# Kernel tuning notes

Hardware: AMD Instinct MI355X
Metric: run time of the kernel (lower is better)

Reference implementation:

```python
import jax, jax.numpy as jnp
from jax import lax
import numpy as np

TOP_PERCENT = 1.3
KSIZE = 3
SIGMA = 0.3 * ((KSIZE - 1) * 0.5 - 1) + 0.8  # torchvision default sigma for ksize=3 -> 0.8


def _gaussian_kernel1d():
    x = jnp.arange(KSIZE, dtype=jnp.float32) - (KSIZE - 1) / 2.0
    k = jnp.exp(-0.5 * (x / SIGMA) ** 2)
    return k / k.sum()


def setup_inputs() -> dict:
    key = jax.random.key(0)
    img = jax.random.uniform(key, (3, 4096, 4096), dtype=jnp.float32)
    return {"img": img}


def reference(img):
    # --- rgb_to_grayscale (ITU-R 601 coefficients, as torchvision) ---
    gray = 0.2989 * img[0] + 0.587 * img[1] + 0.114 * img[2]  # [H, W]

    # --- separable 3x3 gaussian blur, reflect padding (torchvision) ---
    k = _gaussian_kernel1d()
    p = jnp.pad(gray, 1, mode="reflect")  # [H+2, W+2]
    # horizontal pass
    h = k[0] * p[:, :-2] + k[1] * p[:, 1:-1] + k[2] * p[:, 2:]  # [H+2, W]
    # vertical pass
    blur = k[0] * h[:-2, :] + k[1] * h[1:-1, :] + k[2] * h[2:, :]  # [H, W]

    # --- quantile threshold (linear interpolation, matches torch.quantile) ---
    q = (100.0 - TOP_PERCENT) / 100.0
    threshold = jnp.quantile(blur, q)
    mask = (blur >= threshold).astype(jnp.int32)  # [H, W]

    # --- binary opening with 5x5 ones footprint ---
    # erosion = min filter; outside-image treated as 0 (scipy border_value=0),
    # so pad explicitly with zeros and reduce with VALID windows.
    INT_MAX = np.iinfo(np.int32).max
    INT_MIN = np.iinfo(np.int32).min
    padded = jnp.pad(mask, 2)  # zero pad -> borders erode
    eroded = lax.reduce_window(padded, INT_MAX, lax.min, (5, 5), (1, 1), "VALID")
    # dilation = max filter; identity padding (-inf equiv) matches border_value=0
    opened = lax.reduce_window(eroded, INT_MIN, lax.max, (5, 5), (1, 1), "SAME")

    return opened[None, :, :].astype(jnp.int32)  # [1, H, W]
```

## Files before the change

### kernel.cpp

```cpp
#include <hip/hip_runtime.h>
#include <stdint.h>
#include <cmath>


#define HH 4096
#define WW 4096
#define NPIX 16777216u
#define KRANK 16559111u
#define TW 128
#define TH 32

__device__ __forceinline__ unsigned ukey(float v) {
  return (unsigned)(v * 268435456.0f);
}

__global__ __launch_bounds__(256) void k_blur_hist(const float* __restrict__ img,
    float* __restrict__ blur, unsigned* __restrict__ hist1,
    float kn0, float kn1) {
  __shared__ float g[TH + 2][TW + 2];
  __shared__ float hb[TH + 2][TW];
  __shared__ unsigned hist[4096];
  const int tid = threadIdx.x;
  for (int i = tid; i < 4096; i += 256) hist[i] = 0u;

  const int bx = blockIdx.x & 31;
  const int by = blockIdx.x >> 5;
  const int c0 = bx * TW, r0 = by * TH;
  const float* __restrict__ Rp = img;
  const float* __restrict__ Gp = img + (size_t)NPIX;
  const float* __restrict__ Bp = img + 2 * (size_t)NPIX;

  for (int idx = tid; idx < (TH + 2) * (TW + 2); idx += 256) {
    int row = idx / (TW + 2), col = idx - row * (TW + 2);
    int gr = r0 - 1 + row, gc = c0 - 1 + col;
    gr = (gr < 0) ? -gr : ((gr > HH - 1) ? (2 * (HH - 1) - gr) : gr);
    gc = (gc < 0) ? -gc : ((gc > WW - 1) ? (2 * (WW - 1) - gc) : gc);
    size_t o = (size_t)gr * WW + gc;
    float gray = __fadd_rn(__fadd_rn(__fmul_rn(0.2989f, Rp[o]),
                                     __fmul_rn(0.587f, Gp[o])),
                           __fmul_rn(0.114f, Bp[o]));
    g[row][col] = gray;
  }
  __syncthreads();

  for (int idx = tid; idx < (TH + 2) * TW; idx += 256) {
    int row = idx / TW, col = idx - row * TW;
    hb[row][col] = __fadd_rn(__fadd_rn(__fmul_rn(kn0, g[row][col]),
                                       __fmul_rn(kn1, g[row][col + 1])),
                             __fmul_rn(kn0, g[row][col + 2]));
  }
  __syncthreads();

  for (int idx = tid; idx < TH * TW; idx += 256) {
    int row = idx / TW, col = idx - row * TW;
    float v = __fadd_rn(__fadd_rn(__fmul_rn(kn0, hb[row][col]),
                                  __fmul_rn(kn1, hb[row + 1][col])),
                        __fmul_rn(kn0, hb[row + 2][col]));
    blur[(size_t)(r0 + row) * WW + (c0 + col)] = v;
    atomicAdd(&hist[ukey(v) >> 16], 1u);
  }
  __syncthreads();
  for (int i = tid; i < 4096; i += 256) {
    unsigned c = hist[i];
    if (c) atomicAdd(&hist1[i], c);
  }
}

__global__ __launch_bounds__(256) void k_sel1(const unsigned* __restrict__ hist1,
                                              unsigned* __restrict__ sel) {
  __shared__ unsigned part[256];
  const int t = threadIdx.x;
  unsigned loc[16];
  unsigned s = 0;
  for (int i = 0; i < 16; ++i) { loc[i] = hist1[t * 16 + i]; s += loc[i]; }
  part[t] = s;
  __syncthreads();
  for (int off = 1; off < 256; off <<= 1) {
    unsigned v = (t >= off) ? part[t - off] : 0u;
    __syncthreads();
    part[t] += v;
    __syncthreads();
  }
  unsigned incl = part[t], excl = incl - s;
  if (excl <= KRANK && KRANK < incl) {
    unsigned p = excl;
    for (int i = 0; i < 16; ++i) {
      if (KRANK < p + loc[i]) { sel[0] = (unsigned)(t * 16 + i); sel[1] = KRANK - p; break; }
      p += loc[i];
    }
  }
}

__global__ __launch_bounds__(256) void k_hist2(const float4* __restrict__ blur4,
    const unsigned* __restrict__ sel, unsigned* __restrict__ hist2) {
  const unsigned b1 = sel[0];
  size_t i = (size_t)blockIdx.x * 256 + threadIdx.x;
  float4 v = blur4[i];
  unsigned u;
  u = ukey(v.x); if ((u >> 16) == b1) atomicAdd(&hist2[u & 0xFFFFu], 1u);
  u = ukey(v.y); if ((u >> 16) == b1) atomicAdd(&hist2[u & 0xFFFFu], 1u);
  u = ukey(v.z); if ((u >> 16) == b1) atomicAdd(&hist2[u & 0xFFFFu], 1u);
  u = ukey(v.w); if ((u >> 16) == b1) atomicAdd(&hist2[u & 0xFFFFu], 1u);
}

__global__ __launch_bounds__(1024) void k_sel2(const unsigned* __restrict__ hist2,
    const unsigned* __restrict__ sel, float* __restrict__ tptr) {
  __shared__ unsigned part[1024];
  const int t = threadIdx.x;
  const unsigned base = (unsigned)t * 64u;
  unsigned s = 0;
  for (int i = 0; i < 64; ++i) s += hist2[base + i];
  part[t] = s;
  __syncthreads();
  for (int off = 1; off < 1024; off <<= 1) {
    unsigned v = (t >= off) ? part[t - off] : 0u;
    __syncthreads();
    part[t] += v;
    __syncthreads();
  }
  unsigned incl = part[t], excl = incl - s;
  unsigned b1 = sel[0], r1 = sel[1];
  if (excl <= r1 && r1 < incl) {
    unsigned p = excl;
    for (int i = 0; i < 64; ++i) {
      unsigned c = hist2[base + i];
      if (r1 < p + c) {
        unsigned long long ustar = ((unsigned long long)b1 << 16) | (base + i);
        double vv = (double)ustar * (1.0 / 268435456.0);
        *tptr = (float)vv;
        break;
      }
      p += c;
    }
  }
}

__global__ __launch_bounds__(256) void k_mask(const float* __restrict__ blur,
    const float* __restrict__ tptr, unsigned long long* __restrict__ mbits) {
  size_t i = (size_t)blockIdx.x * 256 + threadIdx.x;
  float T = *tptr;
  unsigned long long w = __ballot(blur[i] >= T);
  if ((threadIdx.x & 63) == 0) mbits[i >> 6] = w;
}

__global__ __launch_bounds__(256) void k_erode(
    const unsigned long long* __restrict__ mbits,
    unsigned long long* __restrict__ ebits) {
  int w = blockIdx.x * 256 + threadIdx.x;
  int r = w >> 6, wc = w & 63;
  unsigned long long acc = ~0ull;
  for (int dr = -2; dr <= 2; ++dr) {
    int rr = r + dr;
    unsigned long long h = 0ull;
    if (rr >= 0 && rr <= HH - 1) {
      int rb = (rr << 6) + wc;
      unsigned long long C = mbits[rb];
      unsigned long long L = (wc > 0) ? mbits[rb - 1] : 0ull;
      unsigned long long R = (wc < 63) ? mbits[rb + 1] : 0ull;
      h = C & ((C >> 1) | (R << 63)) & ((C >> 2) | (R << 62))
            & ((C << 1) | (L >> 63)) & ((C << 2) | (L >> 62));
    }
    acc &= h;
  }
  ebits[w] = acc;
}

__global__ __launch_bounds__(256) void k_dilate_out(
    const unsigned long long* __restrict__ ebits, int* __restrict__ out) {
  __shared__ unsigned long long wbuf[256];
  int w = blockIdx.x * 256 + threadIdx.x;
  int r = w >> 6, wc = w & 63;
  unsigned long long acc = 0ull;
  for (int dr = -2; dr <= 2; ++dr) {
    int rr = r + dr;
    if (rr < 0 || rr > HH - 1) continue;
    int rb = (rr << 6) + wc;
    unsigned long long C = ebits[rb];
    unsigned long long L = (wc > 0) ? ebits[rb - 1] : 0ull;
    unsigned long long R = (wc < 63) ? ebits[rb + 1] : 0ull;
    acc |= C | ((C >> 1) | (R << 63)) | ((C >> 2) | (R << 62))
             | ((C << 1) | (L >> 63)) | ((C << 2) | (L >> 62));
  }
  wbuf[threadIdx.x] = acc;
  __syncthreads();
  size_t p0 = (size_t)blockIdx.x * 16384;
  for (int j = threadIdx.x; j < 16384; j += 256)
    out[p0 + j] = (int)((wbuf[j >> 6] >> (j & 63)) & 1ull);
}

extern "C" void kernel_launch(void* const* d_in, const int* in_sizes, int n_in,
                              void* d_out, int out_size, void* d_ws, size_t ws_size,
                              hipStream_t stream) {
  (void)in_sizes; (void)n_in; (void)out_size; (void)ws_size;
  const float* img = (const float*)d_in[0];
  int* out = (int*)d_out;
  char* ws = (char*)d_ws;

  float* blur = (float*)ws;
  unsigned* hist1 = (unsigned*)(ws + 67108864);
  unsigned* hist2 = (unsigned*)(ws + 67108864 + 16384);
  unsigned* sel   = (unsigned*)(ws + 67108864 + 16384 + 262144);
  float* tptr     = (float*)(ws + 67108864 + 16384 + 262144 + 256);
  unsigned long long* mbits =
      (unsigned long long*)(ws + 67108864 + 16384 + 262144 + 512);
  unsigned long long* ebits = mbits + 262144;

  float t = 1.0f / 0.8f;
  float k0 = expf(-0.5f * (t * t));
  float k1 = 1.0f;
  float s = (k0 + k1) + k0;
  float kn0 = k0 / s, kn1 = k1 / s;

  hipMemsetAsync(hist1, 0, 16384 + 262144, stream);
  k_blur_hist<<<4096, 256, 0, stream>>>(img, blur, hist1, kn0, kn1);
  k_sel1<<<1, 256, 0, stream>>>(hist1, sel);
  k_hist2<<<16384, 256, 0, stream>>>((const float4*)blur, sel, hist2);
  k_sel2<<<1, 1024, 0, stream>>>(hist2, sel, tptr);
  k_mask<<<65536, 256, 0, stream>>>(blur, tptr, mbits);
  k_erode<<<1024, 256, 0, stream>>>(mbits, ebits);
  k_dilate_out<<<1024, 256, 0, stream>>>(ebits, out);
}
```

Baseline: 411.1 us.

## Restructure blur as register row streaming and merge histogram pass with masking

The blur kernel drops its shared-memory tiles. Each wavefront now streams rows with float4 loads and computes the horizontal taps through lane shuffles, keeping three rows in registers for the vertical pass. The second histogram pass and the mask pass become one read of the blur buffer: pixels in buckets above the threshold bucket are set directly, and candidates from the threshold bucket go into a bounded list that a small fixup kernel ORs into the mask after selection. The output kernel also writes int4 vectors. This saves one full 64MB read of the blur, but the fixup silently drops candidates if more than CAP fall in the threshold bucket.

```diff
diff --git a/kernel.cpp b/kernel.cpp
--- a/kernel.cpp
+++ b/kernel.cpp
@@ -5,59 +5,91 @@
 
 #define HH 4096
 #define WW 4096
-#define NPIX 16777216u
 #define KRANK 16559111u
-#define TW 128
-#define TH 32
+#define CAP 65536u
 
 __device__ __forceinline__ unsigned ukey(float v) {
   return (unsigned)(v * 268435456.0f);
 }
-
-__global__ __launch_bounds__(256) void k_blur_hist(const float* __restrict__ img,
-    float* __restrict__ blur, unsigned* __restrict__ hist1,
+__device__ __forceinline__ int refl(int i) {
+  return i < 0 ? -i : (i > 4095 ? 8190 - i : i);
+}
+__device__ __forceinline__ float grayf(float r, float g, float b) {
+  return __fadd_rn(__fadd_rn(__fmul_rn(0.2989f, r), __fmul_rn(0.587f, g)),
+                   __fmul_rn(0.114f, b));
+}
+__device__ __forceinline__ float tap3(float a, float b, float c, float kn0, float kn1) {
+  return __fadd_rn(__fadd_rn(__fmul_rn(kn0, a), __fmul_rn(kn1, b)),
+                   __fmul_rn(kn0, c));
+}
+
+__global__ __launch_bounds__(256) void k_blur(const float* __restrict__ img,
+    float4* __restrict__ blur4, unsigned* __restrict__ hist1,
     float kn0, float kn1) {
-  __shared__ float g[TH + 2][TW + 2];
-  __shared__ float hb[TH + 2][TW];
   __shared__ unsigned hist[4096];
   const int tid = threadIdx.x;
   for (int i = tid; i < 4096; i += 256) hist[i] = 0u;
-
-  const int bx = blockIdx.x & 31;
-  const int by = blockIdx.x >> 5;
-  const int c0 = bx * TW, r0 = by * TH;
+  __syncthreads();
+
+  const int lane = tid & 63, wv = tid >> 6;
+  const int bc = (blockIdx.x & 15) << 8;
+  const int r0 = (blockIdx.x >> 4) << 6;
+  const int rstart = r0 + (wv << 4);
   const float* __restrict__ Rp = img;
-  const float* __restrict__ Gp = img + (size_t)NPIX;
-  const float* __restrict__ Bp = img + 2 * (size_t)NPIX;
-
-  for (int idx = tid; idx < (TH + 2) * (TW + 2); idx += 256) {
-    int row = idx / (TW + 2), col = idx - row * (TW + 2);
-    int gr = r0 - 1 + row, gc = c0 - 1 + col;
-    gr = (gr < 0) ? -gr : ((gr > HH - 1) ? (2 * (HH - 1) - gr) : gr);
-    gc = (gc < 0) ? -gc : ((gc > WW - 1) ? (2 * (WW - 1) - gc) : gc);
-    size_t o = (size_t)gr * WW + gc;
-    float gray = __fadd_rn(__fadd_rn(__fmul_rn(0.2989f, Rp[o]),
-                                     __fmul_rn(0.587f, Gp[o])),
-                           __fmul_rn(0.114f, Bp[o]));
-    g[row][col] = gray;
-  }
-  __syncthreads();
-
-  for (int idx = tid; idx < (TH + 2) * TW; idx += 256) {
-    int row = idx / TW, col = idx - row * TW;
-    hb[row][col] = __fadd_rn(__fadd_rn(__fmul_rn(kn0, g[row][col]),
-                                       __fmul_rn(kn1, g[row][col + 1])),
-                             __fmul_rn(kn0, g[row][col + 2]));
-  }
-  __syncthreads();
-
-  for (int idx = tid; idx < TH * TW; idx += 256) {
-    int row = idx / TW, col = idx - row * TW;
-    float v = __fadd_rn(__fadd_rn(__fmul_rn(kn0, hb[row][col]),
-                                  __fmul_rn(kn1, hb[row + 1][col])),
-                        __fmul_rn(kn0, hb[row + 2][col]));
-    blur[(size_t)(r0 + row) * WW + (c0 + col)] = v;
-    atomicAdd(&hist[ukey(v) >> 16], 1u);
+  const float* __restrict__ Gp = img + 16777216;
+  const float* __restrict__ Bp = img + 33554432;
+  const int c4 = bc + (lane << 2);
+
+  auto hrow = [&](int r) -> float4 {
+    const int gr = refl(r);
+    const size_t base = ((size_t)gr << 12) + c4;
+    float4 R = *(const float4*)(Rp + base);
+    float4 G = *(const float4*)(Gp + base);
+    float4 B = *(const float4*)(Bp + base);
+    float4 g;
+    g.x = grayf(R.x, G.x, B.x);
+    g.y = grayf(R.y, G.y, B.y);
+    g.z = grayf(R.z, G.z, B.z);
+    g.w = grayf(R.w, G.w, B.w);
+    float gl = __shfl_up(g.w, 1);
+    float gr_ = __shfl_down(g.x, 1);
+    if (lane == 0) {
+      if (bc == 0) gl = g.y;
+      else {
+        size_t o = ((size_t)gr << 12) + bc - 1;
+        gl = grayf(Rp[o], Gp[o], Bp[o]);
+      }
+    }
+    if (lane == 63) {
+      if (bc == 3840) gr_ = g.z;
+      else {
+        size_t o = ((size_t)gr << 12) + bc + 256;
+        gr_ = grayf(Rp[o], Gp[o], Bp[o]);
+      }
+    }
+    float4 h;
+    h.x = tap3(gl, g.x, g.y, kn0, kn1);
+    h.y = tap3(g.x, g.y, g.z, kn0, kn1);
+    h.z = tap3(g.y, g.z, g.w, kn0, kn1);
+    h.w = tap3(g.z, g.w, gr_, kn0, kn1);
+    return h;
+  };
+
+  float4 h0 = hrow(rstart - 1);
+  float4 h1 = hrow(rstart);
+  for (int i = 0; i < 16; ++i) {
+    float4 h2 = hrow(rstart + 1 + i);
+    float4 v;
+    v.x = tap3(h0.x, h1.x, h2.x, kn0, kn1);
+    v.y = tap3(h0.y, h1.y, h2.y, kn0, kn1);
+    v.z = tap3(h0.z, h1.z, h2.z, kn0, kn1);
+    v.w = tap3(h0.w, h1.w, h2.w, kn0, kn1);
+    blur4[(((size_t)(rstart + i) << 12) + c4) >> 2] = v;
+    atomicAdd(&hist[ukey(v.x) >> 16], 1u);
+    atomicAdd(&hist[ukey(v.y) >> 16], 1u);
+    atomicAdd(&hist[ukey(v.z) >> 16], 1u);
+    atomicAdd(&hist[ukey(v.w) >> 16], 1u);
+    h0 = h1; h1 = h2;
   }
   __syncthreads();
   for (int i = tid; i < 4096; i += 256) {
@@ -91,20 +123,25 @@
   }
 }
 
-__global__ __launch_bounds__(256) void k_hist2(const float4* __restrict__ blur4,
-    const unsigned* __restrict__ sel, unsigned* __restrict__ hist2) {
+__global__ __launch_bounds__(256) void k_pass2(const float* __restrict__ blur,
+    const unsigned* __restrict__ sel, unsigned* __restrict__ hist2,
+    unsigned* __restrict__ cnt, unsigned long long* __restrict__ list,
+    unsigned long long* __restrict__ mbits) {
   const unsigned b1 = sel[0];
-  size_t i = (size_t)blockIdx.x * 256 + threadIdx.x;
-  float4 v = blur4[i];
-  unsigned u;
-  u = ukey(v.x); if ((u >> 16) == b1) atomicAdd(&hist2[u & 0xFFFFu], 1u);
-  u = ukey(v.y); if ((u >> 16) == b1) atomicAdd(&hist2[u & 0xFFFFu], 1u);
-  u = ukey(v.z); if ((u >> 16) == b1) atomicAdd(&hist2[u & 0xFFFFu], 1u);
-  u = ukey(v.w); if ((u >> 16) == b1) atomicAdd(&hist2[u & 0xFFFFu], 1u);
+  const unsigned ub = (b1 + 1u) << 16;
+  unsigned i = blockIdx.x * 256 + threadIdx.x;
+  unsigned u = ukey(blur[i]);
+  unsigned long long w = __ballot(u >= ub);
+  if ((threadIdx.x & 63) == 0) mbits[i >> 6] = w;
+  if ((u >> 16) == b1) {
+    atomicAdd(&hist2[u & 0xFFFFu], 1u);
+    unsigned idx = atomicAdd(cnt, 1u);
+    if (idx < CAP) list[idx] = ((unsigned long long)i << 16) | (u & 0xFFFFu);
+  }
 }
 
 __global__ __launch_bounds__(1024) void k_sel2(const unsigned* __restrict__ hist2,
-    const unsigned* __restrict__ sel, float* __restrict__ tptr) {
+                                               unsigned* __restrict__ sel) {
   __shared__ unsigned part[1024];
   const int t = threadIdx.x;
   const unsigned base = (unsigned)t * 64u;
@@ -119,28 +156,29 @@
     __syncthreads();
   }
   unsigned incl = part[t], excl = incl - s;
-  unsigned b1 = sel[0], r1 = sel[1];
+  unsigned r1 = sel[1];
   if (excl <= r1 && r1 < incl) {
     unsigned p = excl;
     for (int i = 0; i < 64; ++i) {
       unsigned c = hist2[base + i];
-      if (r1 < p + c) {
-        unsigned long long ustar = ((unsigned long long)b1 << 16) | (base + i);
-        double vv = (double)ustar * (1.0 / 268435456.0);
-        *tptr = (float)vv;
-        break;
-      }
+      if (r1 < p + c) { sel[2] = base + i; break; }
       p += c;
     }
   }
 }
 
-__global__ __launch_bounds__(256) void k_mask(const float* __restrict__ blur,
-    const float* __restrict__ tptr, unsigned long long* __restrict__ mbits) {
-  size_t i = (size_t)blockIdx.x * 256 + threadIdx.x;
-  float T = *tptr;
-  unsigned long long w = __ballot(blur[i] >= T);
-  if ((threadIdx.x & 63) == 0) mbits[i >> 6] = w;
+__global__ __launch_bounds__(256) void k_fixup(
+    const unsigned long long* __restrict__ list, const unsigned* __restrict__ cnt,
+    const unsigned* __restrict__ sel, unsigned long long* __restrict__ mbits) {
+  unsigned n = *cnt; if (n > CAP) n = CAP;
+  const unsigned lo = sel[2];
+  for (unsigned j = blockIdx.x * 256 + threadIdx.x; j < n; j += 256 * gridDim.x) {
+    unsigned long long e = list[j];
+    if ((unsigned)(e & 0xFFFFu) >= lo) {
+      unsigned long long pix = e >> 16;
+      atomicOr(&mbits[pix >> 6], 1ull << (pix & 63));
+    }
+  }
 }
 
 __global__ __launch_bounds__(256) void k_erode(
@@ -166,7 +204,7 @@
 }
 
 __global__ __launch_bounds__(256) void k_dilate_out(
-    const unsigned long long* __restrict__ ebits, int* __restrict__ out) {
+    const unsigned long long* __restrict__ ebits, int4* __restrict__ out4) {
   __shared__ unsigned long long wbuf[256];
   int w = blockIdx.x * 256 + threadIdx.x;
   int r = w >> 6, wc = w & 63;
@@ -183,9 +221,12 @@
   }
   wbuf[threadIdx.x] = acc;
   __syncthreads();
-  size_t p0 = (size_t)blockIdx.x * 16384;
-  for (int j = threadIdx.x; j < 16384; j += 256)
-    out[p0 + j] = (int)((wbuf[j >> 6] >> (j & 63)) & 1ull);
+  size_t p0 = (size_t)blockIdx.x * 4096;
+  for (int j = threadIdx.x; j < 4096; j += 256) {
+    unsigned long long word = wbuf[j >> 4];
+    unsigned nib = (unsigned)(word >> ((j & 15) << 2)) & 0xFu;
+    out4[p0 + j] = make_int4(nib & 1, (nib >> 1) & 1, (nib >> 2) & 1, (nib >> 3) & 1);
+  }
 }
 
 extern "C" void kernel_launch(void* const* d_in, const int* in_sizes, int n_in,
@@ -193,17 +234,16 @@
                               hipStream_t stream) {
   (void)in_sizes; (void)n_in; (void)out_size; (void)ws_size;
   const float* img = (const float*)d_in[0];
-  int* out = (int*)d_out;
   char* ws = (char*)d_ws;
 
   float* blur = (float*)ws;
   unsigned* hist1 = (unsigned*)(ws + 67108864);
-  unsigned* hist2 = (unsigned*)(ws + 67108864 + 16384);
-  unsigned* sel   = (unsigned*)(ws + 67108864 + 16384 + 262144);
-  float* tptr     = (float*)(ws + 67108864 + 16384 + 262144 + 256);
-  unsigned long long* mbits =
-      (unsigned long long*)(ws + 67108864 + 16384 + 262144 + 512);
-  unsigned long long* ebits = mbits + 262144;
+  unsigned* hist2 = (unsigned*)(ws + 67125248);
+  unsigned* cnt   = (unsigned*)(ws + 67387392);
+  unsigned* sel   = (unsigned*)(ws + 67387456);
+  unsigned long long* list  = (unsigned long long*)(ws + 67387520);
+  unsigned long long* mbits = (unsigned long long*)(ws + 67911808);
+  unsigned long long* ebits = (unsigned long long*)(ws + 70008960);
 
   float t = 1.0f / 0.8f;
   float k0 = expf(-0.5f * (t * t));
@@ -211,12 +251,12 @@
   float s = (k0 + k1) + k0;
   float kn0 = k0 / s, kn1 = k1 / s;
 
-  hipMemsetAsync(hist1, 0, 16384 + 262144, stream);
-  k_blur_hist<<<4096, 256, 0, stream>>>(img, blur, hist1, kn0, kn1);
+  hipMemsetAsync(hist1, 0, 16384 + 262144 + 64, stream);
+  k_blur<<<1024, 256, 0, stream>>>(img, (float4*)blur, hist1, kn0, kn1);
   k_sel1<<<1, 256, 0, stream>>>(hist1, sel);
-  k_hist2<<<16384, 256, 0, stream>>>((const float4*)blur, sel, hist2);
-  k_sel2<<<1, 1024, 0, stream>>>(hist2, sel, tptr);
-  k_mask<<<65536, 256, 0, stream>>>(blur, tptr, mbits);
+  k_pass2<<<65536, 256, 0, stream>>>(blur, sel, hist2, cnt, list, mbits);
+  k_sel2<<<1, 1024, 0, stream>>>(hist2, sel);
+  k_fixup<<<32, 256, 0, stream>>>(list, cnt, sel, mbits);
   k_erode<<<1024, 256, 0, stream>>>(mbits, ebits);
-  k_dilate_out<<<1024, 256, 0, stream>>>(ebits, out);
-}
+  k_dilate_out<<<1024, 256, 0, stream>>>(ebits, (int4*)d_out);
+}
```

After: 371.5 us. 9.6% less time.
